# Optimization experiments

Measured on AMD Instinct MI355X. Metric: run time of the kernel, lower is better.

## Reference

```python
import jax, jax.numpy as jnp
import numpy as np

E = 1024
H = 16
HD = E // H  # 64


def setup_inputs() -> dict:
    key = jax.random.key(0)
    ks = jax.random.split(key, 5)
    x = jax.random.normal(ks[0], (2, 2048, E), dtype=jnp.float32)
    s = 1.0 / np.sqrt(E)
    W_qkv = jax.random.uniform(ks[1], (E, 3 * E), jnp.float32, -s, s)
    b_qkv = jax.random.uniform(ks[2], (3 * E,), jnp.float32, -s, s)
    W_out = jax.random.uniform(ks[3], (E, E), jnp.float32, -s, s)
    b_out = jax.random.uniform(ks[4], (E,), jnp.float32, -s, s)
    return {"x": x, "W_qkv": W_qkv, "b_qkv": b_qkv, "W_out": W_out, "b_out": b_out}


def reference(x, W_qkv, b_qkv, W_out, b_out):
    B, N, _ = x.shape
    scale = HD ** (-0.5)
    qkv = x @ W_qkv + b_qkv                         # [B, N, 3E]
    qkv = qkv.reshape(B, N, H, 3 * HD)              # torch layout: per-head 3*hd chunk
    qkv = qkv.transpose(0, 2, 1, 3)                 # [B, H, N, 3*hd]
    q, k, v = jnp.split(qkv, 3, axis=-1)            # each [B, H, N, hd]
    attn = jnp.einsum('bhqd,bhkd->bhqk', q, k) * scale
    attn = jax.nn.softmax(attn, axis=-1)            # dropout is identity in eval
    out = jnp.einsum('bhqk,bhkd->bhqd', attn, v)    # [B, H, N, hd]
    out = out.transpose(0, 2, 1, 3).reshape(B, N, E)
    return out @ W_out + b_out
```

## Files before the change

kernel.cpp:

```cpp
#include <hip/hip_runtime.h>


#define SEQ 2048
#define NH  16

typedef __attribute__((ext_vector_type(8))) short short8;
typedef __attribute__((ext_vector_type(4))) short short4v;
typedef __attribute__((ext_vector_type(4))) float floatx4;
typedef __attribute__((ext_vector_type(4))) _Float16 half4;
typedef __attribute__((ext_vector_type(2))) _Float16 half2v;
typedef __attribute__((ext_vector_type(2))) __fp16 fp16x2;

#define QSCALE 0.1803368801111204f

__device__ __forceinline__ short f2bf(float f) {
    union { float f; unsigned u; } v; v.f = f;
    unsigned r = v.u + 0x7fffu + ((v.u >> 16) & 1u);
    return (short)(r >> 16);
}

__device__ __forceinline__ float fast_exp2(float x) {
#if __has_builtin(__builtin_amdgcn_exp2f)
    return __builtin_amdgcn_exp2f(x);
#else
    return exp2f(x);
#endif
}

__device__ __forceinline__ half2v cvt_pk(float a, float b) {
#if __has_builtin(__builtin_amdgcn_cvt_pkrtz)
    union { fp16x2 i; half2v o; } u;
    u.i = __builtin_amdgcn_cvt_pkrtz(a, b);
    return u.o;
#else
    half2v r; r.x = (_Float16)a; r.y = (_Float16)b; return r;
#endif
}

#define GLDS16(gp, lp)                                                          \
    __builtin_amdgcn_global_load_lds(                                           \
        (const __attribute__((address_space(1))) unsigned int*)(gp),            \
        (__attribute__((address_space(3))) unsigned int*)(lp), 16, 0, 0)

__global__ __launch_bounds__(256) void cast_f32_bf16_kernel(
    const float* __restrict__ in, short* __restrict__ out)
{
    int i = blockIdx.x * 256 + threadIdx.x;
    const float4* in4 = (const float4*)in + (size_t)i * 2;
    float4 a = in4[0], b = in4[1];
    short8 o = { f2bf(a.x), f2bf(a.y), f2bf(a.z), f2bf(a.w),
                 f2bf(b.x), f2bf(b.y), f2bf(b.z), f2bf(b.w) };
    *((short8*)out + i) = o;
}

__global__ __launch_bounds__(256) void transpose_cast_kernel(
    const float* __restrict__ in, short* __restrict__ out, int R, int C)
{
    __shared__ float T[64][65];
    const int tid = threadIdx.x;
    const int c0 = blockIdx.x * 64, r0 = blockIdx.y * 64;
#pragma unroll
    for (int it = 0; it < 4; ++it) {
        int r = it * 16 + (tid >> 4), c = (tid & 15) * 4;
        float4 v = *(const float4*)(in + (size_t)(r0 + r) * C + c0 + c);
        T[c+0][r] = v.x; T[c+1][r] = v.y; T[c+2][r] = v.z; T[c+3][r] = v.w;
    }
    __syncthreads();
#pragma unroll
    for (int it = 0; it < 4; ++it) {
        int oc = it * 16 + (tid >> 4), k = (tid & 15) * 4;
        short4v o = { f2bf(T[oc][k]), f2bf(T[oc][k+1]), f2bf(T[oc][k+2]), f2bf(T[oc][k+3]) };
        *(short4v*)(out + (size_t)(c0 + oc) * R + r0 + k) = o;
    }
}

__global__ __launch_bounds__(256) void vtrans_kernel(
    const _Float16* __restrict__ vn, _Float16* __restrict__ vt)
{
    __shared__ _Float16 T[64][72];
    const int tid = threadIdx.x;
    const int bh = blockIdx.y, n0 = blockIdx.x * 64;
#pragma unroll
    for (int it = 0; it < 2; ++it) {
        int n = it * 32 + (tid >> 3), c = (tid & 7) * 8;
        const _Float16* p = vn + ((size_t)bh * SEQ + n0 + n) * 64 + c;
        half4 a = *(const half4*)(p);
        half4 b = *(const half4*)(p + 4);
        T[c+0][n] = a.x; T[c+1][n] = a.y; T[c+2][n] = a.z; T[c+3][n] = a.w;
        T[c+4][n] = b.x; T[c+5][n] = b.y; T[c+6][n] = b.z; T[c+7][n] = b.w;
    }
    __syncthreads();
#pragma unroll
    for (int it = 0; it < 2; ++it) {
        int d = it * 32 + (tid >> 3), cn = (tid & 7) * 8;
        half4 o0 = { T[d][cn+0], T[d][cn+1], T[d][cn+2], T[d][cn+3] };
        half4 o1 = { T[d][cn+4], T[d][cn+5], T[d][cn+6], T[d][cn+7] };
        _Float16* q = vt + ((size_t)bh * 64 + d) * SEQ + n0 + cn;
        *(half4*)(q)     = o0;
        *(half4*)(q + 4) = o1;
    }
}

#define GEMM_CORE(A_PTR, B_PTR, LDA, LDB)                                        \
    __shared__ short As[128 * 32];                                               \
    __shared__ short Bs[128 * 32];                                               \
    const int tid  = threadIdx.x;                                                \
    const int lane = tid & 63, w = tid >> 6;                                     \
    const int quad = lane >> 4, l16 = lane & 15;                                 \
    const int wm = w >> 1, wn = w & 1;                                           \
    const int c0 = blockIdx.x * 128, r0 = blockIdx.y * 128;                      \
    floatx4 acc[4][4];                                                           \
    _Pragma("unroll")                                                            \
    for (int i = 0; i < 4; ++i)                                                  \
        _Pragma("unroll")                                                        \
        for (int j = 0; j < 4; ++j) acc[i][j] = (floatx4){0.f, 0.f, 0.f, 0.f};   \
    const int srow = tid >> 2;                                                   \
    const int sgx  = ((tid & 3) ^ ((srow >> 1) & 3)) * 8;                        \
    const short* Ag = (A_PTR) + (size_t)(r0 + srow) * (LDA) + sgx;               \
    const short* Bg = (B_PTR) + (size_t)(c0 + srow) * (LDB) + sgx;               \
    const int fsw = (l16 >> 1) & 3;                                              \
    for (int kk = 0; kk < 1024; kk += 32) {                                      \
        __syncthreads();                                                         \
        GLDS16(Ag + kk,                      As + tid * 8);                      \
        GLDS16(Ag + (size_t)64 * (LDA) + kk, As + 2048 + tid * 8);               \
        GLDS16(Bg + kk,                      Bs + tid * 8);                      \
        GLDS16(Bg + (size_t)64 * (LDB) + kk, Bs + 2048 + tid * 8);               \
        __syncthreads();                                                         \
        short8 af[4], bf[4];                                                     \
        _Pragma("unroll")                                                        \
        for (int mt = 0; mt < 4; ++mt)                                           \
            af[mt] = *(const short8*)&As[(wm * 64 + mt * 16 + l16) * 32 + (quad ^ fsw) * 8]; \
        _Pragma("unroll")                                                        \
        for (int nt = 0; nt < 4; ++nt)                                           \
            bf[nt] = *(const short8*)&Bs[(wn * 64 + nt * 16 + l16) * 32 + (quad ^ fsw) * 8]; \
        _Pragma("unroll")                                                        \
        for (int mt = 0; mt < 4; ++mt)                                           \
            _Pragma("unroll")                                                    \
            for (int nt = 0; nt < 4; ++nt)                                       \
                acc[mt][nt] = __builtin_amdgcn_mfma_f32_16x16x32_bf16(           \
                    af[mt], bf[nt], acc[mt][nt], 0, 0, 0);                       \
    }

__global__ __launch_bounds__(256) void qkv_gemm_kernel(
    const short* __restrict__ xb, const short* __restrict__ wt,
    const float* __restrict__ bias,
    short* __restrict__ qb, short* __restrict__ kb, _Float16* __restrict__ vnb)
{
    GEMM_CORE(xb, wt, 1024, 1024)
#pragma unroll
    for (int nt = 0; nt < 4; ++nt) {
        int gc = c0 + wn * 64 + nt * 16 + l16;
        int head = gc / 192;
        int t = (gc - head * 192) >> 6;
        int d = gc & 63;
        float bv = bias[gc];
#pragma unroll
        for (int mt = 0; mt < 4; ++mt) {
#pragma unroll
            for (int reg = 0; reg < 4; ++reg) {
                int tok = r0 + wm * 64 + mt * 16 + quad * 4 + reg;
                int bh = (tok >> 11) * NH + head;
                int n = tok & (SEQ - 1);
                float val = acc[mt][nt][reg] + bv;
                if (t == 0)      qb[((size_t)bh * SEQ + n) * 64 + d] = f2bf(val * QSCALE);
                else if (t == 1) kb[((size_t)bh * SEQ + n) * 64 + d] = f2bf(val);
                else             vnb[((size_t)bh * SEQ + n) * 64 + d] = (_Float16)val;
            }
        }
    }
}

__global__ __launch_bounds__(512) void out_gemm_kernel(
    const short* __restrict__ ab, const short* __restrict__ wt,
    const float* __restrict__ bias, float* __restrict__ out)
{
    __shared__ short As[128 * 32];
    __shared__ short Bs[128 * 32];
    const int tid  = threadIdx.x;
    const int lane = tid & 63, w = tid >> 6;
    const int quad = lane >> 4, l16 = lane & 15;
    const int wm = w >> 2, wn = w & 3;
    const int c0 = blockIdx.x * 128, r0 = blockIdx.y * 128;
    floatx4 acc[4][2];
#pragma unroll
    for (int i = 0; i < 4; ++i)
#pragma unroll
        for (int j = 0; j < 2; ++j) acc[i][j] = (floatx4){0.f, 0.f, 0.f, 0.f};
    const int srow = tid >> 2;
    const int sgx  = ((tid & 3) ^ ((srow >> 1) & 3)) * 8;
    const short* Ag = ab + (size_t)(r0 + srow) * 1024 + sgx;
    const short* Bg = wt + (size_t)(c0 + srow) * 1024 + sgx;
    const int fsw = (l16 >> 1) & 3;
    for (int kk = 0; kk < 1024; kk += 32) {
        __syncthreads();
        GLDS16(Ag + kk, As + tid * 8);
        GLDS16(Bg + kk, Bs + tid * 8);
        __syncthreads();
        short8 af[4], bf[2];
#pragma unroll
        for (int mt = 0; mt < 4; ++mt)
            af[mt] = *(const short8*)&As[(wm * 64 + mt * 16 + l16) * 32 + (quad ^ fsw) * 8];
#pragma unroll
        for (int nt = 0; nt < 2; ++nt)
            bf[nt] = *(const short8*)&Bs[(wn * 32 + nt * 16 + l16) * 32 + (quad ^ fsw) * 8];
#pragma unroll
        for (int mt = 0; mt < 4; ++mt)
#pragma unroll
            for (int nt = 0; nt < 2; ++nt)
                acc[mt][nt] = __builtin_amdgcn_mfma_f32_16x16x32_bf16(
                    af[mt], bf[nt], acc[mt][nt], 0, 0, 0);
    }
#pragma unroll
    for (int nt = 0; nt < 2; ++nt) {
        int gc = c0 + wn * 32 + nt * 16 + l16;
        float bv = bias[gc];
#pragma unroll
        for (int mt = 0; mt < 4; ++mt) {
#pragma unroll
            for (int reg = 0; reg < 4; ++reg) {
                int tok = r0 + wm * 64 + mt * 16 + quad * 4 + reg;
                out[(size_t)tok * 1024 + gc] = acc[mt][nt][reg] + bv;
            }
        }
    }
}

__global__ __launch_bounds__(256) void attn_kernel(
    const short* __restrict__ qb, const short* __restrict__ kb,
    const _Float16* __restrict__ vtb, short* __restrict__ ob)
{
    __shared__ short   Ks[128 * 64];
    __shared__ _Float16 Vts[64 * 128];
    const int tid  = threadIdx.x;
    const int lane = tid & 63, w = tid >> 6;
    const int quad = lane >> 4, l16 = lane & 15;
    const int bh = blockIdx.x;
    const int q0 = blockIdx.y * 64;

    const short* qp = qb + ((size_t)bh * SEQ + q0 + w * 16 + l16) * 64 + quad * 8;
    const short8 aq0 = *(const short8*)(qp);
    const short8 aq1 = *(const short8*)(qp + 32);

    const int krow = tid >> 3, kg = tid & 7;
    const short* kgp = kb + ((size_t)bh * SEQ + krow) * 64 + (kg ^ (krow & 7)) * 8;
    const int vrow = tid >> 4, vg = tid & 15;
    const _Float16* vgp = vtb + ((size_t)bh * 64 + vrow) * SEQ + (vg ^ (vrow & 7)) * 8;

    floatx4 o_acc[4];
#pragma unroll
    for (int dt = 0; dt < 4; ++dt) o_acc[dt] = (floatx4){0.f, 0.f, 0.f, 0.f};
    float l_run = 0.f;
    const int fsw = l16 & 7;

    for (int k0 = 0; k0 < SEQ; k0 += 128) {
        __syncthreads();
        const short* kc_p = kgp + (size_t)k0 * 64;
        GLDS16(kc_p,        Ks + tid * 8);
        GLDS16(kc_p + 2048, Ks + 2048 + tid * 8);
        GLDS16(kc_p + 4096, Ks + 4096 + tid * 8);
        GLDS16(kc_p + 6144, Ks + 6144 + tid * 8);
        const _Float16* vc_p = vgp + k0;
        GLDS16(vc_p,                     (short*)Vts + tid * 8);
        GLDS16(vc_p + (size_t)16 * SEQ,  (short*)Vts + 2048 + tid * 8);
        GLDS16(vc_p + (size_t)32 * SEQ,  (short*)Vts + 4096 + tid * 8);
        GLDS16(vc_p + (size_t)48 * SEQ,  (short*)Vts + 6144 + tid * 8);
        __syncthreads();

        floatx4 sacc[8];
#pragma unroll
        for (int kt = 0; kt < 8; ++kt) sacc[kt] = (floatx4){0.f, 0.f, 0.f, 0.f};
#pragma unroll
        for (int kt = 0; kt < 8; ++kt) {
            short8 ak0 = *(const short8*)&Ks[(kt * 16 + l16) * 64 + ((0 + quad) ^ fsw) * 8];
            short8 ak1 = *(const short8*)&Ks[(kt * 16 + l16) * 64 + ((4 + quad) ^ fsw) * 8];
            sacc[kt] = __builtin_amdgcn_mfma_f32_16x16x32_bf16(ak0, aq0, sacc[kt], 0, 0, 0);
            sacc[kt] = __builtin_amdgcn_mfma_f32_16x16x32_bf16(ak1, aq1, sacc[kt], 0, 0, 0);
        }

        half4 pf[8];
        float psum = 0.f;
#pragma unroll
        for (int kt = 0; kt < 8; ++kt) {
            float p0 = fast_exp2(sacc[kt][0]);
            float p1 = fast_exp2(sacc[kt][1]);
            float p2 = fast_exp2(sacc[kt][2]);
            float p3 = fast_exp2(sacc[kt][3]);
            psum += (p0 + p1) + (p2 + p3);
            half2v lo = cvt_pk(p0, p1), hi = cvt_pk(p2, p3);
            pf[kt] = (half4){lo.x, lo.y, hi.x, hi.y};
        }
        l_run += psum;

#pragma unroll
        for (int kt = 0; kt < 8; ++kt) {
            const int gb = kt * 2 + (quad >> 1);
#pragma unroll
            for (int dt = 0; dt < 4; ++dt) {
                half4 av = *(const half4*)&Vts[(dt * 16 + l16) * 128 + (gb ^ fsw) * 8 + (quad & 1) * 4];
                o_acc[dt] = __builtin_amdgcn_mfma_f32_16x16x16f16(av, pf[kt], o_acc[dt], 0, 0, 0);
            }
        }
    }

    l_run += __shfl_xor(l_run, 16);
    l_run += __shfl_xor(l_run, 32);
    float inv = 1.0f / l_run;

    const int b = bh >> 4, h = bh & 15;
    int tok = b * SEQ + q0 + w * 16 + l16;
#pragma unroll
    for (int dt = 0; dt < 4; ++dt) {
        short4v o4 = { f2bf(o_acc[dt][0] * inv), f2bf(o_acc[dt][1] * inv),
                       f2bf(o_acc[dt][2] * inv), f2bf(o_acc[dt][3] * inv) };
        *(short4v*)(ob + (size_t)tok * 1024 + h * 64 + dt * 16 + quad * 4) = o4;
    }
}

extern "C" void kernel_launch(void* const* d_in, const int* in_sizes, int n_in,
                              void* d_out, int out_size, void* d_ws, size_t ws_size,
                              hipStream_t stream) {
    const float* x     = (const float*)d_in[0];
    const float* W_qkv = (const float*)d_in[1];
    const float* b_qkv = (const float*)d_in[2];
    const float* W_out = (const float*)d_in[3];
    const float* b_out = (const float*)d_in[4];
    float* out = (float*)d_out;

    short* xb      = (short*)d_ws;
    short* wqkvt   = xb    + (size_t)4096 * 1024;
    short* woutt   = wqkvt + (size_t)3072 * 1024;
    short* qb      = woutt + (size_t)1024 * 1024;
    short* kb      = qb    + (size_t)32 * SEQ * 64;
    _Float16* vnb  = (_Float16*)(kb + (size_t)32 * SEQ * 64);
    _Float16* vtb  = vnb + (size_t)32 * SEQ * 64;
    short* ob      = (short*)(vtb + (size_t)32 * 64 * SEQ);

    cast_f32_bf16_kernel<<<2048, 256, 0, stream>>>(x, xb);
    transpose_cast_kernel<<<dim3(48, 16), 256, 0, stream>>>(W_qkv, wqkvt, 1024, 3072);
    transpose_cast_kernel<<<dim3(16, 16), 256, 0, stream>>>(W_out, woutt, 1024, 1024);
    qkv_gemm_kernel<<<dim3(24, 32), 256, 0, stream>>>(xb, wqkvt, b_qkv, qb, kb, vnb);
    vtrans_kernel<<<dim3(32, 32), 256, 0, stream>>>(vnb, vtb);
    attn_kernel<<<dim3(32, 32), 256, 0, stream>>>(qb, kb, vtb, ob);
    out_gemm_kernel<<<dim3(8, 32), 512, 0, stream>>>(ob, woutt, b_out, out);
}
```

Baseline: 205.5 us.

## Split attention across waves by key range with register-streamed K/V and LDS reduction

The attention kernel no longer has each wave own 16 queries and stage K/V tiles through shared memory. Each wave now handles all 64 queries over its own slice of keys, loading K and V fragments straight from global memory into registers with double buffering. Partial outputs and row sums are then reduced across waves through LDS. This removes per-tile barriers and LDS staging, at the cost of more registers (launch bounds set to 2 blocks), a cross-wave reduction at the end, and uncoalesced-looking global fragment loads. The V transpose write-out is also reorganised to read LDS rows as vectors.

```diff
diff --git a/kernel.cpp b/kernel.cpp
--- a/kernel.cpp
+++ b/kernel.cpp
@@ -92,12 +92,14 @@
     __syncthreads();
 #pragma unroll
     for (int it = 0; it < 2; ++it) {
-        int d = it * 32 + (tid >> 3), cn = (tid & 7) * 8;
-        half4 o0 = { T[d][cn+0], T[d][cn+1], T[d][cn+2], T[d][cn+3] };
-        half4 o1 = { T[d][cn+4], T[d][cn+5], T[d][cn+6], T[d][cn+7] };
-        _Float16* q = vt + ((size_t)bh * 64 + d) * SEQ + n0 + cn;
-        *(half4*)(q)     = o0;
-        *(half4*)(q + 4) = o1;
+        int idx = it * 256 + tid;
+        int quad = idx & 3, d = (idx >> 2) & 63, u = idx >> 8;
+        const _Float16* row = &T[d][u * 32 + quad * 4];
+        half4 lo = *(const half4*)(row);
+        half4 hi = *(const half4*)(row + 16);
+        _Float16* q = vt + ((size_t)bh * 64 + d) * SEQ + n0 + u * 32 + quad * 8;
+        *(half4*)(q)     = lo;
+        *(half4*)(q + 4) = hi;
     }
 }
 
@@ -225,94 +227,145 @@
     }
 }
 
-__global__ __launch_bounds__(256) void attn_kernel(
+__device__ __forceinline__ void attn_load(
+    short8 (&ak)[4], short8 (&av)[4],
+    const short* __restrict__ kp, const short* __restrict__ vp, int it)
+{
+#pragma unroll
+    for (int kt = 0; kt < 2; ++kt)
+#pragma unroll
+        for (int kc = 0; kc < 2; ++kc)
+            ak[kt * 2 + kc] = *(const short8*)(kp + (size_t)it * 8192 + kt * 1024 + kc * 32);
+#pragma unroll
+    for (int dt = 0; dt < 4; ++dt)
+        av[dt] = *(const short8*)(vp + (size_t)dt * (16 * SEQ) + it * 128);
+}
+
+__device__ __forceinline__ void attn_step(
+    const short8 (&ak)[4], const short8 (&av)[4],
+    const short8 (&aq)[4][2], floatx4 (&o_acc)[4][4], float (&lw)[4])
+{
+    floatx4 sacc[2][4];
+#pragma unroll
+    for (int kt = 0; kt < 2; ++kt)
+#pragma unroll
+        for (int qf = 0; qf < 4; ++qf) {
+            floatx4 z = (floatx4){0.f, 0.f, 0.f, 0.f};
+            z = __builtin_amdgcn_mfma_f32_16x16x32_bf16(ak[kt * 2 + 0], aq[qf][0], z, 0, 0, 0);
+            sacc[kt][qf] = __builtin_amdgcn_mfma_f32_16x16x32_bf16(ak[kt * 2 + 1], aq[qf][1], z, 0, 0, 0);
+        }
+    half4 pf[2][4];
+#pragma unroll
+    for (int kt = 0; kt < 2; ++kt)
+#pragma unroll
+        for (int qf = 0; qf < 4; ++qf) {
+            float p0 = fast_exp2(sacc[kt][qf][0]);
+            float p1 = fast_exp2(sacc[kt][qf][1]);
+            float p2 = fast_exp2(sacc[kt][qf][2]);
+            float p3 = fast_exp2(sacc[kt][qf][3]);
+            lw[qf] += (p0 + p1) + (p2 + p3);
+            half2v lo = cvt_pk(p0, p1), hi = cvt_pk(p2, p3);
+            pf[kt][qf] = (half4){lo.x, lo.y, hi.x, hi.y};
+        }
+#pragma unroll
+    for (int dt = 0; dt < 4; ++dt) {
+        union { short8 s; struct { half4 lo; half4 hi; } h; } u;
+        u.s = av[dt];
+#pragma unroll
+        for (int qf = 0; qf < 4; ++qf) {
+            o_acc[dt][qf] = __builtin_amdgcn_mfma_f32_16x16x16f16(u.h.lo, pf[0][qf], o_acc[dt][qf], 0, 0, 0);
+            o_acc[dt][qf] = __builtin_amdgcn_mfma_f32_16x16x16f16(u.h.hi, pf[1][qf], o_acc[dt][qf], 0, 0, 0);
+        }
+    }
+}
+
+__global__ __launch_bounds__(256, 2) void attn_kernel(
     const short* __restrict__ qb, const short* __restrict__ kb,
     const _Float16* __restrict__ vtb, short* __restrict__ ob)
 {
-    __shared__ short   Ks[128 * 64];
-    __shared__ _Float16 Vts[64 * 128];
+    __shared__ float RedA[4096];
+    __shared__ float RedB[4096];
+    __shared__ float Ls[4][64];
     const int tid  = threadIdx.x;
     const int lane = tid & 63, w = tid >> 6;
     const int quad = lane >> 4, l16 = lane & 15;
     const int bh = blockIdx.x;
     const int q0 = blockIdx.y * 64;
 
-    const short* qp = qb + ((size_t)bh * SEQ + q0 + w * 16 + l16) * 64 + quad * 8;
-    const short8 aq0 = *(const short8*)(qp);
-    const short8 aq1 = *(const short8*)(qp + 32);
-
-    const int krow = tid >> 3, kg = tid & 7;
-    const short* kgp = kb + ((size_t)bh * SEQ + krow) * 64 + (kg ^ (krow & 7)) * 8;
-    const int vrow = tid >> 4, vg = tid & 15;
-    const _Float16* vgp = vtb + ((size_t)bh * 64 + vrow) * SEQ + (vg ^ (vrow & 7)) * 8;
-
-    floatx4 o_acc[4];
-#pragma unroll
-    for (int dt = 0; dt < 4; ++dt) o_acc[dt] = (floatx4){0.f, 0.f, 0.f, 0.f};
-    float l_run = 0.f;
-    const int fsw = l16 & 7;
-
-    for (int k0 = 0; k0 < SEQ; k0 += 128) {
-        __syncthreads();
-        const short* kc_p = kgp + (size_t)k0 * 64;
-        GLDS16(kc_p,        Ks + tid * 8);
-        GLDS16(kc_p + 2048, Ks + 2048 + tid * 8);
-        GLDS16(kc_p + 4096, Ks + 4096 + tid * 8);
-        GLDS16(kc_p + 6144, Ks + 6144 + tid * 8);
-        const _Float16* vc_p = vgp + k0;
-        GLDS16(vc_p,                     (short*)Vts + tid * 8);
-        GLDS16(vc_p + (size_t)16 * SEQ,  (short*)Vts + 2048 + tid * 8);
-        GLDS16(vc_p + (size_t)32 * SEQ,  (short*)Vts + 4096 + tid * 8);
-        GLDS16(vc_p + (size_t)48 * SEQ,  (short*)Vts + 6144 + tid * 8);
-        __syncthreads();
-
-        floatx4 sacc[8];
-#pragma unroll
-        for (int kt = 0; kt < 8; ++kt) sacc[kt] = (floatx4){0.f, 0.f, 0.f, 0.f};
-#pragma unroll
-        for (int kt = 0; kt < 8; ++kt) {
-            short8 ak0 = *(const short8*)&Ks[(kt * 16 + l16) * 64 + ((0 + quad) ^ fsw) * 8];
-            short8 ak1 = *(const short8*)&Ks[(kt * 16 + l16) * 64 + ((4 + quad) ^ fsw) * 8];
-            sacc[kt] = __builtin_amdgcn_mfma_f32_16x16x32_bf16(ak0, aq0, sacc[kt], 0, 0, 0);
-            sacc[kt] = __builtin_amdgcn_mfma_f32_16x16x32_bf16(ak1, aq1, sacc[kt], 0, 0, 0);
-        }
-
-        half4 pf[8];
-        float psum = 0.f;
-#pragma unroll
-        for (int kt = 0; kt < 8; ++kt) {
-            float p0 = fast_exp2(sacc[kt][0]);
-            float p1 = fast_exp2(sacc[kt][1]);
-            float p2 = fast_exp2(sacc[kt][2]);
-            float p3 = fast_exp2(sacc[kt][3]);
-            psum += (p0 + p1) + (p2 + p3);
-            half2v lo = cvt_pk(p0, p1), hi = cvt_pk(p2, p3);
-            pf[kt] = (half4){lo.x, lo.y, hi.x, hi.y};
-        }
-        l_run += psum;
-
-#pragma unroll
-        for (int kt = 0; kt < 8; ++kt) {
-            const int gb = kt * 2 + (quad >> 1);
-#pragma unroll
-            for (int dt = 0; dt < 4; ++dt) {
-                half4 av = *(const half4*)&Vts[(dt * 16 + l16) * 128 + (gb ^ fsw) * 8 + (quad & 1) * 4];
-                o_acc[dt] = __builtin_amdgcn_mfma_f32_16x16x16f16(av, pf[kt], o_acc[dt], 0, 0, 0);
+    short8 aq[4][2];
+#pragma unroll
+    for (int qf = 0; qf < 4; ++qf) {
+        const short* qp = qb + ((size_t)bh * SEQ + q0 + qf * 16 + l16) * 64 + quad * 8;
+        aq[qf][0] = *(const short8*)(qp);
+        aq[qf][1] = *(const short8*)(qp + 32);
+    }
+
+    const short* kp = kb + ((size_t)bh * SEQ + w * 32 + l16) * 64 + quad * 8;
+    const short* vp = (const short*)vtb + ((size_t)bh * 64 + l16) * SEQ + w * 32 + quad * 8;
+
+    floatx4 o_acc[4][4];
+#pragma unroll
+    for (int dt = 0; dt < 4; ++dt)
+#pragma unroll
+        for (int qf = 0; qf < 4; ++qf) o_acc[dt][qf] = (floatx4){0.f, 0.f, 0.f, 0.f};
+    float lw[4] = {0.f, 0.f, 0.f, 0.f};
+
+    short8 akA[4], avA[4], akB[4], avB[4];
+    attn_load(akA, avA, kp, vp, 0);
+    for (int it = 0; it < 16; it += 2) {
+        attn_load(akB, avB, kp, vp, it + 1);
+        attn_step(akA, avA, aq, o_acc, lw);
+        int nn = (it + 2 < 16) ? it + 2 : 0;
+        attn_load(akA, avA, kp, vp, nn);
+        attn_step(akB, avB, aq, o_acc, lw);
+    }
+
+#pragma unroll
+    for (int qf = 0; qf < 4; ++qf) {
+        lw[qf] += __shfl_xor(lw[qf], 16);
+        lw[qf] += __shfl_xor(lw[qf], 32);
+        if (quad == 0) Ls[w][qf * 16 + l16] = lw[qf];
+    }
+
+#pragma unroll
+    for (int dt = 0; dt < 4; ++dt)
+#pragma unroll
+        for (int qf = 0; qf < 4; ++qf) {
+            int fi = (((dt * 4 + qf) * 4 + quad) * 16 + l16) * 4;
+            if (w == 1) *(floatx4*)&RedA[fi] = o_acc[dt][qf];
+            if (w == 3) *(floatx4*)&RedB[fi] = o_acc[dt][qf];
+        }
+    __syncthreads();
+    if (w == 0 || w == 2) {
+#pragma unroll
+        for (int dt = 0; dt < 4; ++dt)
+#pragma unroll
+            for (int qf = 0; qf < 4; ++qf) {
+                int fi = (((dt * 4 + qf) * 4 + quad) * 16 + l16) * 4;
+                o_acc[dt][qf] += *(const floatx4*)((w == 0) ? &RedA[fi] : &RedB[fi]);
+                if (w == 2) *(floatx4*)&RedB[fi] = o_acc[dt][qf];
             }
-        }
-    }
-
-    l_run += __shfl_xor(l_run, 16);
-    l_run += __shfl_xor(l_run, 32);
-    float inv = 1.0f / l_run;
-
-    const int b = bh >> 4, h = bh & 15;
-    int tok = b * SEQ + q0 + w * 16 + l16;
-#pragma unroll
-    for (int dt = 0; dt < 4; ++dt) {
-        short4v o4 = { f2bf(o_acc[dt][0] * inv), f2bf(o_acc[dt][1] * inv),
-                       f2bf(o_acc[dt][2] * inv), f2bf(o_acc[dt][3] * inv) };
-        *(short4v*)(ob + (size_t)tok * 1024 + h * 64 + dt * 16 + quad * 4) = o4;
+    }
+    __syncthreads();
+    if (w == 0) {
+        float inv[4];
+#pragma unroll
+        for (int qf = 0; qf < 4; ++qf) {
+            int qi = qf * 16 + l16;
+            inv[qf] = 1.0f / (Ls[0][qi] + Ls[1][qi] + Ls[2][qi] + Ls[3][qi]);
+        }
+        const int b = bh >> 4, h = bh & 15;
+#pragma unroll
+        for (int dt = 0; dt < 4; ++dt)
+#pragma unroll
+            for (int qf = 0; qf < 4; ++qf) {
+                int fi = (((dt * 4 + qf) * 4 + quad) * 16 + l16) * 4;
+                floatx4 o = o_acc[dt][qf] + *(const floatx4*)&RedB[fi];
+                int tok = b * SEQ + q0 + qf * 16 + l16;
+                short4v o4 = { f2bf(o[0] * inv[qf]), f2bf(o[1] * inv[qf]),
+                               f2bf(o[2] * inv[qf]), f2bf(o[3] * inv[qf]) };
+                *(short4v*)(ob + (size_t)tok * 1024 + h * 64 + dt * 16 + quad * 4) = o4;
+            }
     }
 }
 
```

New measurement: 221.7 us. +7.9%, slower.
